# Performance work log

Hardware: AMD Instinct MI355X
Metric: run time of the kernel (lower is better)

Reference implementation:

```python
import math
import jax, jax.numpy as jnp
import numpy as np

B, T, C, H = 2, 4096, 512, 8  # batch, seq_len, n_embd, n_head
D = C // H                    # head_dim = 64

def setup_inputs() -> dict:
    key = jax.random.key(0)
    k1, k2, k3 = jax.random.split(key, 3)
    x = jax.random.normal(k1, (B, T, C), dtype=jnp.float32)
    # torch Linear(C, 3C, bias=False): y = x @ W.T; we store the transposed
    # weight directly so the forward is x @ W_attn.
    W_attn = jax.random.normal(k2, (C, 3 * C), dtype=jnp.float32) * 0.02
    W_proj = jax.random.normal(k3, (C, C), dtype=jnp.float32) * 0.02
    return {"x": x, "W_attn": W_attn, "W_proj": W_proj}

def reference(x, W_attn, W_proj):
    b, t, c = x.shape
    # fused QKV projection, split like .split(n_embd, dim=2)
    qkv = x @ W_attn                              # [B,T,3C]
    q, k, v = jnp.split(qkv, 3, axis=-1)          # each [B,T,C]
    def to_heads(u):
        return u.reshape(b, t, H, D).transpose(0, 2, 1, 3)  # [B,H,T,D]
    q, k, v = to_heads(q), to_heads(k), to_heads(v)
    scale = 1.0 / math.sqrt(D)
    att = jnp.einsum('bhqd,bhkd->bhqk', q, k) * scale       # [B,H,T,T]
    causal = jnp.tril(jnp.ones((t, t), dtype=bool))         # masked_fill(triu(...,1), -inf)
    att = jnp.where(causal, att, -jnp.inf)
    probs = jax.nn.softmax(att, axis=-1)
    y = jnp.einsum('bhqk,bhkd->bhqd', probs, v)             # [B,H,T,D]
    y = y.transpose(0, 2, 1, 3).reshape(b, t, c)            # [B,T,C]
    return y @ W_proj
```

## Files before the change

kernel.cpp:

```cpp
#include <hip/hip_runtime.h>
#include <hip/hip_bf16.h>
#include <stdint.h>


typedef __attribute__((ext_vector_type(8))) short short8;
typedef __attribute__((ext_vector_type(4))) float floatx4;

__device__ __forceinline__ unsigned short f2bf(float f) {
    unsigned int x = __float_as_uint(f);
    unsigned int r = x + 0x7fffu + ((x >> 16) & 1u);
    return (unsigned short)(r >> 16);
}

__device__ __forceinline__ unsigned int pk_bf16(float a, float b) {
    __hip_bfloat162 p = __float22bfloat162_rn(make_float2(a, b));
    return *reinterpret_cast<unsigned int*>(&p);
}

__global__ __launch_bounds__(256) void prep_a(
    const float* __restrict__ x, unsigned short* __restrict__ xb,
    const float* __restrict__ Wa, unsigned short* __restrict__ WaT)
{
    const int bid = blockIdx.x;
    const int tid = threadIdx.x;
    if (bid < 2048) {
        size_t i = ((size_t)bid * 256 + tid) * 8;
        float4 a = *reinterpret_cast<const float4*>(x + i);
        float4 b = *reinterpret_cast<const float4*>(x + i + 4);
        unsigned short o[8] = {f2bf(a.x), f2bf(a.y), f2bf(a.z), f2bf(a.w),
                               f2bf(b.x), f2bf(b.y), f2bf(b.z), f2bf(b.w)};
        *reinterpret_cast<uint4*>(xb + i) = *reinterpret_cast<uint4*>(o);
    } else {
        __shared__ unsigned short tile[32][34];
        const int t2 = bid - 2048;
        const int n0 = (t2 % 48) * 32, k0 = (t2 / 48) * 32;
        const int tx = tid & 31, ty = tid >> 5;
        #pragma unroll
        for (int p = 0; p < 4; ++p)
            tile[tx][ty + p * 8] = f2bf(Wa[(size_t)(k0 + ty + p * 8) * 1536 + n0 + tx]);
        __syncthreads();
        #pragma unroll
        for (int p = 0; p < 4; ++p)
            WaT[(size_t)(n0 + ty + p * 8) * 512 + k0 + tx] = tile[ty + p * 8][tx];
    }
}

__global__ __launch_bounds__(256) void transpose_wp(
    const float* __restrict__ W, unsigned short* __restrict__ Wt)
{
    __shared__ unsigned short tile[32][34];
    const int tid = threadIdx.x;
    const int tx = tid & 31, ty = tid >> 5;
    const int n0 = blockIdx.x * 32, k0 = blockIdx.y * 32;
    #pragma unroll
    for (int p = 0; p < 4; ++p)
        tile[tx][ty + p * 8] = f2bf(W[(size_t)(k0 + ty + p * 8) * 512 + n0 + tx]);
    __syncthreads();
    #pragma unroll
    for (int p = 0; p < 4; ++p)
        Wt[(size_t)(n0 + ty + p * 8) * 512 + k0 + tx] = tile[ty + p * 8][tx];
}

template<int EPI>
__global__ __launch_bounds__(256) void mm_bt(
    const unsigned short* __restrict__ A,
    const unsigned short* __restrict__ Bt,
    void* __restrict__ outp)
{
    __shared__ __align__(16) unsigned char smem[40960];

    const int tid  = threadIdx.x;
    const int wave = tid >> 6;
    const int lane = tid & 63;
    const int quad = lane >> 4;
    const int l16  = lane & 15;
    const int wr   = wave >> 1;
    const int wc   = wave & 1;
    const int m0 = blockIdx.x * 128;
    const int n0 = blockIdx.y * 128;

    floatx4 acc[4][4];
    #pragma unroll
    for (int i = 0; i < 4; ++i)
        #pragma unroll
        for (int j = 0; j < 4; ++j) acc[i][j] = (floatx4){0.f, 0.f, 0.f, 0.f};

    const int row = tid >> 1;
    const int cb  = (tid & 1) * 16;

    const unsigned short* ap = &A[(size_t)(m0 + row) * 512 + cb];
    const unsigned short* bp = &Bt[(size_t)(n0 + row) * 512 + cb];

    uint4 ra0 = *reinterpret_cast<const uint4*>(ap);
    uint4 ra1 = *reinterpret_cast<const uint4*>(ap + 8);
    uint4 rb0 = *reinterpret_cast<const uint4*>(bp);
    uint4 rb1 = *reinterpret_cast<const uint4*>(bp + 8);
    {
        auto Al = reinterpret_cast<unsigned short(*)[40]>(smem);
        auto Bl = reinterpret_cast<unsigned short(*)[40]>(smem + 10240);
        *reinterpret_cast<uint4*>(&Al[row][cb])     = ra0;
        *reinterpret_cast<uint4*>(&Al[row][cb + 8]) = ra1;
        *reinterpret_cast<uint4*>(&Bl[row][cb])     = rb0;
        *reinterpret_cast<uint4*>(&Bl[row][cb + 8]) = rb1;
    }

    for (int it = 0; it < 16; ++it) {
        __syncthreads();
        const int k0 = it * 32;
        if (it < 15) {
            ra0 = *reinterpret_cast<const uint4*>(ap + k0 + 32);
            ra1 = *reinterpret_cast<const uint4*>(ap + k0 + 40);
            rb0 = *reinterpret_cast<const uint4*>(bp + k0 + 32);
            rb1 = *reinterpret_cast<const uint4*>(bp + k0 + 40);
        }

        auto Al = reinterpret_cast<unsigned short(*)[40]>(smem + (it & 1) * 20480);
        auto Bl = reinterpret_cast<unsigned short(*)[40]>(smem + (it & 1) * 20480 + 10240);

        short8 af[4], bf[4];
        #pragma unroll
        for (int ti = 0; ti < 4; ++ti)
            af[ti] = *reinterpret_cast<const short8*>(&Al[wr * 64 + ti * 16 + l16][quad * 8]);
        #pragma unroll
        for (int tj = 0; tj < 4; ++tj)
            bf[tj] = *reinterpret_cast<const short8*>(&Bl[wc * 64 + tj * 16 + l16][quad * 8]);
        #pragma unroll
        for (int ti = 0; ti < 4; ++ti)
            #pragma unroll
            for (int tj = 0; tj < 4; ++tj)
                acc[ti][tj] = __builtin_amdgcn_mfma_f32_16x16x32_bf16(af[ti], bf[tj], acc[ti][tj], 0, 0, 0);

        if (it < 15) {
            auto An = reinterpret_cast<unsigned short(*)[40]>(smem + ((it + 1) & 1) * 20480);
            auto Bn = reinterpret_cast<unsigned short(*)[40]>(smem + ((it + 1) & 1) * 20480 + 10240);
            *reinterpret_cast<uint4*>(&An[row][cb])     = ra0;
            *reinterpret_cast<uint4*>(&An[row][cb + 8]) = ra1;
            *reinterpret_cast<uint4*>(&Bn[row][cb])     = rb0;
            *reinterpret_cast<uint4*>(&Bn[row][cb + 8]) = rb1;
        }
    }

    if (EPI == 0) {
        unsigned short* WS = (unsigned short*)outp;
        unsigned short* Qb  = WS;
        unsigned short* Kb  = WS + 4194304;
        unsigned short* Vtb = WS + 8388608;
        const int which = n0 >> 9;
        const int h = ((n0 + wc * 64) >> 6) & 7;

        if (which == 2) {
            auto Tr = reinterpret_cast<unsigned short(*)[80]>(smem);
            __syncthreads();
            #pragma unroll
            for (int ti = 0; ti < 4; ++ti)
                #pragma unroll
                for (int tj = 0; tj < 4; ++tj) {
                    unsigned int lo = pk_bf16(acc[ti][tj][0], acc[ti][tj][1]);
                    unsigned int hi = pk_bf16(acc[ti][tj][2], acc[ti][tj][3]);
                    *reinterpret_cast<uint2*>(&Tr[(wave << 6) + tj * 16 + l16][ti * 16 + quad * 4])
                        = make_uint2(lo, hi);
                }
            const int b = m0 >> 12;
            const int bh = b * 8 + h;
            const int t0g = (m0 & 4095) + wr * 64;
            const int tseg = (lane & 7) * 8;
            #pragma unroll
            for (int p = 0; p < 8; ++p) {
                int dl = p * 8 + (lane >> 3);
                uint4 v = *reinterpret_cast<const uint4*>(&Tr[(wave << 6) + dl][tseg]);
                *reinterpret_cast<uint4*>(&Vtb[((size_t)(bh * 64 + dl)) * 4096 + t0g + tseg]) = v;
            }
        } else {
            const float sc = (which == 0) ? 0.18033688f : 1.0f;
            #pragma unroll
            for (int ti = 0; ti < 4; ++ti) {
                #pragma unroll
                for (int r = 0; r < 4; ++r) {
                    int m = m0 + wr * 64 + ti * 16 + quad * 4 + r;
                    int b = m >> 12, t = m & 4095;
                    int bh = b * 8 + h;
                    #pragma unroll
                    for (int tj = 0; tj < 4; ++tj) {
                        int d = tj * 16 + l16;
                        unsigned short val = f2bf(acc[ti][tj][r] * sc);
                        if (which == 0) Qb[((size_t)bh * 4096 + t) * 64 + d] = val;
                        else            Kb[((size_t)bh * 4096 + t) * 64 + d] = val;
                    }
                }
            }
        }
    } else {
        float* Out = (float*)outp;
        #pragma unroll
        for (int ti = 0; ti < 4; ++ti) {
            #pragma unroll
            for (int r = 0; r < 4; ++r) {
                int m = m0 + wr * 64 + ti * 16 + quad * 4 + r;
                #pragma unroll
                for (int tj = 0; tj < 4; ++tj) {
                    int n = n0 + wc * 64 + tj * 16 + l16;
                    Out[(size_t)m * 512 + n] = acc[ti][tj][r];
                }
            }
        }
    }
}

__global__ __launch_bounds__(256) void attn_mfma(
    const unsigned short* __restrict__ Q,
    const unsigned short* __restrict__ K,
    const unsigned short* __restrict__ Vt,
    unsigned short* __restrict__ Y)
{
    __shared__ __align__(16) unsigned short Kc[2][64][72];
    __shared__ __align__(16) unsigned short Vc[2][64][72];
    __shared__ __align__(16) unsigned short Pc[4][16][72];

    const int tid  = threadIdx.x;
    const int wave = tid >> 6;
    const int lane = tid & 63;
    const int quad = lane >> 4;
    const int l16  = lane & 15;

    const int bid = blockIdx.x;
    const int bh = bid & 15;
    const int j  = (bid >> 4) & 15;
    const int g  = bid >> 8;
    const int qb = (g == 0) ? j : (g == 1) ? (63 - j) : (g == 2) ? (16 + j) : (47 - j);
    const int m0 = qb * 64;

    const unsigned short* Qp = Q  + (size_t)bh * (4096 * 64);
    const unsigned short* Kp = K  + (size_t)bh * (4096 * 64);
    const unsigned short* Vp = Vt + (size_t)bh * (64 * 4096);

    const int qrow = m0 + wave * 16 + l16;
    short8 qf[2];
    qf[0] = *reinterpret_cast<const short8*>(&Qp[(size_t)qrow * 64 + quad * 8]);
    qf[1] = *reinterpret_cast<const short8*>(&Qp[(size_t)qrow * 64 + 32 + quad * 8]);

    short8 ones;
    #pragma unroll
    for (int i = 0; i < 8; ++i) ones[i] = (short)0x3F80;

    floatx4 o[4] = {{0,0,0,0},{0,0,0,0},{0,0,0,0},{0,0,0,0}};
    floatx4 o4 = {0, 0, 0, 0};

    const int r0 = tid >> 3,          c0 = (tid & 7) * 8;
    const int r1 = (tid + 256) >> 3,  c1 = c0;

    uint4 rk0 = *reinterpret_cast<const uint4*>(&Kp[(size_t)r0 * 64 + c0]);
    uint4 rk1 = *reinterpret_cast<const uint4*>(&Kp[(size_t)r1 * 64 + c1]);
    uint4 rv0 = *reinterpret_cast<const uint4*>(&Vp[(size_t)r0 * 4096 + c0]);
    uint4 rv1 = *reinterpret_cast<const uint4*>(&Vp[(size_t)r1 * 4096 + c1]);
    *reinterpret_cast<uint4*>(&Kc[0][r0][c0]) = rk0;
    *reinterpret_cast<uint4*>(&Kc[0][r1][c1]) = rk1;
    *reinterpret_cast<uint4*>(&Vc[0][r0][c0]) = rv0;
    *reinterpret_cast<uint4*>(&Vc[0][r1][c1]) = rv1;

    for (int kt = 0; kt <= qb; ++kt) {
        __syncthreads();
        const int cur = kt & 1;
        const int nxt = cur ^ 1;

        if (kt < qb) {
            const int jn = (kt + 1) * 64;
            rk0 = *reinterpret_cast<const uint4*>(&Kp[(size_t)(jn + r0) * 64 + c0]);
            rk1 = *reinterpret_cast<const uint4*>(&Kp[(size_t)(jn + r1) * 64 + c1]);
            rv0 = *reinterpret_cast<const uint4*>(&Vp[(size_t)r0 * 4096 + jn + c0]);
            rv1 = *reinterpret_cast<const uint4*>(&Vp[(size_t)r1 * 4096 + jn + c1]);
        }

        float sv[4][4];
        #pragma unroll
        for (int ct = 0; ct < 4; ++ct) {
            floatx4 s = {0, 0, 0, 0};
            #pragma unroll
            for (int kk = 0; kk < 2; ++kk) {
                short8 a = *reinterpret_cast<const short8*>(&Kc[cur][ct * 16 + l16][kk * 32 + quad * 8]);
                s = __builtin_amdgcn_mfma_f32_16x16x32_bf16(a, qf[kk], s, 0, 0, 0);
            }
            sv[ct][0] = s[0]; sv[ct][1] = s[1]; sv[ct][2] = s[2]; sv[ct][3] = s[3];
        }

        if (kt == qb) {
            #pragma unroll
            for (int ct = 0; ct < 4; ++ct)
                #pragma unroll
                for (int r = 0; r < 4; ++r) {
                    int keyl = ct * 16 + quad * 4 + r;
                    int ql   = wave * 16 + l16;
                    sv[ct][r] = (keyl <= ql) ? sv[ct][r] : -1e30f;
                }
        }
        #pragma unroll
        for (int ct = 0; ct < 4; ++ct)
            #pragma unroll
            for (int r = 0; r < 4; ++r)
                sv[ct][r] = __builtin_amdgcn_exp2f(sv[ct][r]);

        #pragma unroll
        for (int ct = 0; ct < 4; ++ct) {
            unsigned int d0 = pk_bf16(sv[ct][0], sv[ct][1]);
            unsigned int d1 = pk_bf16(sv[ct][2], sv[ct][3]);
            *reinterpret_cast<uint2*>(&Pc[wave][l16][ct * 16 + quad * 4]) = make_uint2(d0, d1);
        }

        short8 pa[2];
        pa[0] = *reinterpret_cast<const short8*>(&Pc[wave][l16][quad * 8]);
        pa[1] = *reinterpret_cast<const short8*>(&Pc[wave][l16][32 + quad * 8]);

        #pragma unroll
        for (int kk = 0; kk < 2; ++kk)
            o4 = __builtin_amdgcn_mfma_f32_16x16x32_bf16(pa[kk], ones, o4, 0, 0, 0);
        #pragma unroll
        for (int n = 0; n < 4; ++n) {
            #pragma unroll
            for (int kk = 0; kk < 2; ++kk) {
                short8 b = *reinterpret_cast<const short8*>(&Vc[cur][n * 16 + l16][kk * 32 + quad * 8]);
                o[n] = __builtin_amdgcn_mfma_f32_16x16x32_bf16(pa[kk], b, o[n], 0, 0, 0);
            }
        }

        if (kt < qb) {
            *reinterpret_cast<uint4*>(&Kc[nxt][r0][c0]) = rk0;
            *reinterpret_cast<uint4*>(&Kc[nxt][r1][c1]) = rk1;
            *reinterpret_cast<uint4*>(&Vc[nxt][r0][c0]) = rv0;
            *reinterpret_cast<uint4*>(&Vc[nxt][r1][c1]) = rv1;
        }
    }

    const int b = bh >> 3, h = bh & 7;
    #pragma unroll
    for (int r = 0; r < 4; ++r) {
        float inv = 1.0f / o4[r];
        int t = m0 + wave * 16 + quad * 4 + r;
        #pragma unroll
        for (int n = 0; n < 4; ++n)
            Y[((size_t)(b * 4096 + t)) * 512 + h * 64 + n * 16 + l16] = f2bf(o[n][r] * inv);
    }
}

extern "C" void kernel_launch(void* const* d_in, const int* in_sizes, int n_in,
                              void* d_out, int out_size, void* d_ws, size_t ws_size,
                              hipStream_t stream) {
    const float* x  = (const float*)d_in[0];
    const float* Wa = (const float*)d_in[1];
    const float* Wp = (const float*)d_in[2];
    float* out = (float*)d_out;
    unsigned short* ws = (unsigned short*)d_ws;

    unsigned short* Qb  = ws;
    unsigned short* Kb  = ws + 4194304;
    unsigned short* Vtb = ws + 8388608;
    unsigned short* Yb  = ws + 12582912;
    unsigned short* WaT = Yb;
    unsigned short* WpT = Qb;
    unsigned short* xb  = (unsigned short*)d_out;

    prep_a<<<dim3(2816), dim3(256), 0, stream>>>(x, xb, Wa, WaT);
    mm_bt<0><<<dim3(64, 12), dim3(256), 0, stream>>>(xb, WaT, (void*)ws);
    attn_mfma<<<dim3(1024), dim3(256), 0, stream>>>(Qb, Kb, Vtb, Yb);
    transpose_wp<<<dim3(16, 16), dim3(256), 0, stream>>>(Wp, WpT);
    mm_bt<1><<<dim3(64, 4), dim3(256), 0, stream>>>(Yb, WpT, (void*)out);
}
```

Baseline: 171.8 us.

## Enlarge attention query tile to 128 rows with XOR-swizzled LDS

Each attention block now handles 128 query rows instead of 64: each wave covers two 16-row query tiles, so every K/V tile loaded into LDS is reused across twice as many queries and the grid halves. Padded shared arrays are replaced with unpadded 64-wide rows using an XOR swizzle on the 8-element column chunks to avoid bank conflicts. Waves skip key tiles past their diagonal, which adds divergence between waves in the final tiles and raises register pressure from doubled accumulators. With only 512 blocks, occupancy and load balance across CUs may suffer.

```diff
diff --git a/kernel.cpp b/kernel.cpp
--- a/kernel.cpp
+++ b/kernel.cpp
@@ -212,132 +212,156 @@
     const unsigned short* __restrict__ Vt,
     unsigned short* __restrict__ Y)
 {
-    __shared__ __align__(16) unsigned short Kc[2][64][72];
-    __shared__ __align__(16) unsigned short Vc[2][64][72];
-    __shared__ __align__(16) unsigned short Pc[4][16][72];
+    __shared__ __align__(16) unsigned short Kc[2][64][64];
+    __shared__ __align__(16) unsigned short Vc[2][64][64];
+    __shared__ __align__(16) unsigned short Pc[4][32][64];
 
     const int tid  = threadIdx.x;
     const int wave = tid >> 6;
     const int lane = tid & 63;
     const int quad = lane >> 4;
     const int l16  = lane & 15;
+    const int swz  = l16 & 7;
 
     const int bid = blockIdx.x;
-    const int bh = bid & 15;
-    const int j  = (bid >> 4) & 15;
-    const int g  = bid >> 8;
-    const int qb = (g == 0) ? j : (g == 1) ? (63 - j) : (g == 2) ? (16 + j) : (47 - j);
-    const int m0 = qb * 64;
+    const int bh  = bid & 15;
+    const int j   = (bid >> 4) & 15;
+    const int g   = bid >> 8;
+    const int qb  = (g == 0) ? j : (31 - j);
+    const int m0  = qb * 128;
 
     const unsigned short* Qp = Q  + (size_t)bh * (4096 * 64);
     const unsigned short* Kp = K  + (size_t)bh * (4096 * 64);
     const unsigned short* Vp = Vt + (size_t)bh * (64 * 4096);
 
-    const int qrow = m0 + wave * 16 + l16;
-    short8 qf[2];
-    qf[0] = *reinterpret_cast<const short8*>(&Qp[(size_t)qrow * 64 + quad * 8]);
-    qf[1] = *reinterpret_cast<const short8*>(&Qp[(size_t)qrow * 64 + 32 + quad * 8]);
+    short8 qf[2][2];
+    #pragma unroll
+    for (int qt = 0; qt < 2; ++qt) {
+        const size_t qr = (size_t)(m0 + wave * 32 + qt * 16 + l16) * 64;
+        qf[qt][0] = *reinterpret_cast<const short8*>(&Qp[qr + quad * 8]);
+        qf[qt][1] = *reinterpret_cast<const short8*>(&Qp[qr + 32 + quad * 8]);
+    }
 
     short8 ones;
     #pragma unroll
     for (int i = 0; i < 8; ++i) ones[i] = (short)0x3F80;
 
-    floatx4 o[4] = {{0,0,0,0},{0,0,0,0},{0,0,0,0},{0,0,0,0}};
-    floatx4 o4 = {0, 0, 0, 0};
-
-    const int r0 = tid >> 3,          c0 = (tid & 7) * 8;
-    const int r1 = (tid + 256) >> 3,  c1 = c0;
+    floatx4 o[2][4];
+    #pragma unroll
+    for (int qt = 0; qt < 2; ++qt)
+        #pragma unroll
+        for (int n = 0; n < 4; ++n) o[qt][n] = (floatx4){0.f, 0.f, 0.f, 0.f};
+    floatx4 o4[2] = {{0, 0, 0, 0}, {0, 0, 0, 0}};
+
+    const int r0 = tid >> 3;
+    const int r1 = r0 + 32;
+    const int cc = tid & 7;
+    const int c0 = cc * 8;
+    const int sc = ((cc ^ (r0 & 7)) << 3);
 
     uint4 rk0 = *reinterpret_cast<const uint4*>(&Kp[(size_t)r0 * 64 + c0]);
-    uint4 rk1 = *reinterpret_cast<const uint4*>(&Kp[(size_t)r1 * 64 + c1]);
+    uint4 rk1 = *reinterpret_cast<const uint4*>(&Kp[(size_t)r1 * 64 + c0]);
     uint4 rv0 = *reinterpret_cast<const uint4*>(&Vp[(size_t)r0 * 4096 + c0]);
-    uint4 rv1 = *reinterpret_cast<const uint4*>(&Vp[(size_t)r1 * 4096 + c1]);
-    *reinterpret_cast<uint4*>(&Kc[0][r0][c0]) = rk0;
-    *reinterpret_cast<uint4*>(&Kc[0][r1][c1]) = rk1;
-    *reinterpret_cast<uint4*>(&Vc[0][r0][c0]) = rv0;
-    *reinterpret_cast<uint4*>(&Vc[0][r1][c1]) = rv1;
-
-    for (int kt = 0; kt <= qb; ++kt) {
+    uint4 rv1 = *reinterpret_cast<const uint4*>(&Vp[(size_t)r1 * 4096 + c0]);
+    *reinterpret_cast<uint4*>(&Kc[0][r0][sc]) = rk0;
+    *reinterpret_cast<uint4*>(&Kc[0][r1][sc]) = rk1;
+    *reinterpret_cast<uint4*>(&Vc[0][r0][sc]) = rv0;
+    *reinterpret_cast<uint4*>(&Vc[0][r1][sc]) = rv1;
+
+    const int nt   = 2 * qb + 2;
+    const int diag = 2 * qb + (wave >> 1);
+
+    for (int kt = 0; kt < nt; ++kt) {
         __syncthreads();
         const int cur = kt & 1;
         const int nxt = cur ^ 1;
 
-        if (kt < qb) {
+        if (kt + 1 < nt) {
             const int jn = (kt + 1) * 64;
             rk0 = *reinterpret_cast<const uint4*>(&Kp[(size_t)(jn + r0) * 64 + c0]);
-            rk1 = *reinterpret_cast<const uint4*>(&Kp[(size_t)(jn + r1) * 64 + c1]);
+            rk1 = *reinterpret_cast<const uint4*>(&Kp[(size_t)(jn + r1) * 64 + c0]);
             rv0 = *reinterpret_cast<const uint4*>(&Vp[(size_t)r0 * 4096 + jn + c0]);
-            rv1 = *reinterpret_cast<const uint4*>(&Vp[(size_t)r1 * 4096 + jn + c1]);
-        }
-
-        float sv[4][4];
-        #pragma unroll
-        for (int ct = 0; ct < 4; ++ct) {
-            floatx4 s = {0, 0, 0, 0};
-            #pragma unroll
-            for (int kk = 0; kk < 2; ++kk) {
-                short8 a = *reinterpret_cast<const short8*>(&Kc[cur][ct * 16 + l16][kk * 32 + quad * 8]);
-                s = __builtin_amdgcn_mfma_f32_16x16x32_bf16(a, qf[kk], s, 0, 0, 0);
-            }
-            sv[ct][0] = s[0]; sv[ct][1] = s[1]; sv[ct][2] = s[2]; sv[ct][3] = s[3];
-        }
-
-        if (kt == qb) {
-            #pragma unroll
-            for (int ct = 0; ct < 4; ++ct)
-                #pragma unroll
-                for (int r = 0; r < 4; ++r) {
-                    int keyl = ct * 16 + quad * 4 + r;
-                    int ql   = wave * 16 + l16;
-                    sv[ct][r] = (keyl <= ql) ? sv[ct][r] : -1e30f;
-                }
-        }
-        #pragma unroll
-        for (int ct = 0; ct < 4; ++ct)
-            #pragma unroll
-            for (int r = 0; r < 4; ++r)
-                sv[ct][r] = __builtin_amdgcn_exp2f(sv[ct][r]);
-
-        #pragma unroll
-        for (int ct = 0; ct < 4; ++ct) {
-            unsigned int d0 = pk_bf16(sv[ct][0], sv[ct][1]);
-            unsigned int d1 = pk_bf16(sv[ct][2], sv[ct][3]);
-            *reinterpret_cast<uint2*>(&Pc[wave][l16][ct * 16 + quad * 4]) = make_uint2(d0, d1);
-        }
-
-        short8 pa[2];
-        pa[0] = *reinterpret_cast<const short8*>(&Pc[wave][l16][quad * 8]);
-        pa[1] = *reinterpret_cast<const short8*>(&Pc[wave][l16][32 + quad * 8]);
-
-        #pragma unroll
-        for (int kk = 0; kk < 2; ++kk)
-            o4 = __builtin_amdgcn_mfma_f32_16x16x32_bf16(pa[kk], ones, o4, 0, 0, 0);
-        #pragma unroll
-        for (int n = 0; n < 4; ++n) {
-            #pragma unroll
-            for (int kk = 0; kk < 2; ++kk) {
-                short8 b = *reinterpret_cast<const short8*>(&Vc[cur][n * 16 + l16][kk * 32 + quad * 8]);
-                o[n] = __builtin_amdgcn_mfma_f32_16x16x32_bf16(pa[kk], b, o[n], 0, 0, 0);
-            }
-        }
-
-        if (kt < qb) {
-            *reinterpret_cast<uint4*>(&Kc[nxt][r0][c0]) = rk0;
-            *reinterpret_cast<uint4*>(&Kc[nxt][r1][c1]) = rk1;
-            *reinterpret_cast<uint4*>(&Vc[nxt][r0][c0]) = rv0;
-            *reinterpret_cast<uint4*>(&Vc[nxt][r1][c1]) = rv1;
+            rv1 = *reinterpret_cast<const uint4*>(&Vp[(size_t)r1 * 4096 + jn + c0]);
+        }
+
+        if (kt <= diag) {
+            const bool dg = (kt == diag);
+            #pragma unroll
+            for (int ct = 0; ct < 4; ++ct) {
+                const unsigned short* kr = &Kc[cur][ct * 16 + l16][0];
+                short8 a0 = *reinterpret_cast<const short8*>(kr + ((quad ^ swz) << 3));
+                short8 a1 = *reinterpret_cast<const short8*>(kr + (((4 + quad) ^ swz) << 3));
+                #pragma unroll
+                for (int qt = 0; qt < 2; ++qt) {
+                    floatx4 s = {0, 0, 0, 0};
+                    s = __builtin_amdgcn_mfma_f32_16x16x32_bf16(a0, qf[qt][0], s, 0, 0, 0);
+                    s = __builtin_amdgcn_mfma_f32_16x16x32_bf16(a1, qf[qt][1], s, 0, 0, 0);
+                    float sv[4];
+                    #pragma unroll
+                    for (int r = 0; r < 4; ++r) sv[r] = s[r];
+                    if (dg) {
+                        const int ql = (wave & 1) * 32 + qt * 16 + l16;
+                        #pragma unroll
+                        for (int r = 0; r < 4; ++r) {
+                            int keyl = ct * 16 + quad * 4 + r;
+                            sv[r] = (keyl <= ql) ? sv[r] : -1e30f;
+                        }
+                    }
+                    #pragma unroll
+                    for (int r = 0; r < 4; ++r) sv[r] = __builtin_amdgcn_exp2f(sv[r]);
+                    unsigned int d0 = pk_bf16(sv[0], sv[1]);
+                    unsigned int d1 = pk_bf16(sv[2], sv[3]);
+                    *reinterpret_cast<uint2*>(
+                        &Pc[wave][qt * 16 + l16]
+                           [(((ct * 2 + (quad >> 1)) ^ swz) << 3) + (quad & 1) * 4])
+                        = make_uint2(d0, d1);
+                }
+            }
+
+            short8 pa[2][2];
+            #pragma unroll
+            for (int qt = 0; qt < 2; ++qt) {
+                const unsigned short* pr = &Pc[wave][qt * 16 + l16][0];
+                pa[qt][0] = *reinterpret_cast<const short8*>(pr + ((quad ^ swz) << 3));
+                pa[qt][1] = *reinterpret_cast<const short8*>(pr + (((4 + quad) ^ swz) << 3));
+            }
+            #pragma unroll
+            for (int qt = 0; qt < 2; ++qt) {
+                o4[qt] = __builtin_amdgcn_mfma_f32_16x16x32_bf16(pa[qt][0], ones, o4[qt], 0, 0, 0);
+                o4[qt] = __builtin_amdgcn_mfma_f32_16x16x32_bf16(pa[qt][1], ones, o4[qt], 0, 0, 0);
+            }
+            #pragma unroll
+            for (int n = 0; n < 4; ++n) {
+                const unsigned short* vr = &Vc[cur][n * 16 + l16][0];
+                short8 b0 = *reinterpret_cast<const short8*>(vr + ((quad ^ swz) << 3));
+                short8 b1 = *reinterpret_cast<const short8*>(vr + (((4 + quad) ^ swz) << 3));
+                #pragma unroll
+                for (int qt = 0; qt < 2; ++qt) {
+                    o[qt][n] = __builtin_amdgcn_mfma_f32_16x16x32_bf16(pa[qt][0], b0, o[qt][n], 0, 0, 0);
+                    o[qt][n] = __builtin_amdgcn_mfma_f32_16x16x32_bf16(pa[qt][1], b1, o[qt][n], 0, 0, 0);
+                }
+            }
+        }
+
+        if (kt + 1 < nt) {
+            *reinterpret_cast<uint4*>(&Kc[nxt][r0][sc]) = rk0;
+            *reinterpret_cast<uint4*>(&Kc[nxt][r1][sc]) = rk1;
+            *reinterpret_cast<uint4*>(&Vc[nxt][r0][sc]) = rv0;
+            *reinterpret_cast<uint4*>(&Vc[nxt][r1][sc]) = rv1;
         }
     }
 
     const int b = bh >> 3, h = bh & 7;
     #pragma unroll
-    for (int r = 0; r < 4; ++r) {
-        float inv = 1.0f / o4[r];
-        int t = m0 + wave * 16 + quad * 4 + r;
-        #pragma unroll
-        for (int n = 0; n < 4; ++n)
-            Y[((size_t)(b * 4096 + t)) * 512 + h * 64 + n * 16 + l16] = f2bf(o[n][r] * inv);
-    }
+    for (int qt = 0; qt < 2; ++qt)
+        #pragma unroll
+        for (int r = 0; r < 4; ++r) {
+            float inv = 1.0f / o4[qt][r];
+            int t = m0 + wave * 32 + qt * 16 + quad * 4 + r;
+            #pragma unroll
+            for (int n = 0; n < 4; ++n)
+                Y[((size_t)(b * 4096 + t)) * 512 + h * 64 + n * 16 + l16] = f2bf(o[qt][n][r] * inv);
+        }
 }
 
 extern "C" void kernel_launch(void* const* d_in, const int* in_sizes, int n_in,
@@ -359,7 +383,7 @@
 
     prep_a<<<dim3(2816), dim3(256), 0, stream>>>(x, xb, Wa, WaT);
     mm_bt<0><<<dim3(64, 12), dim3(256), 0, stream>>>(xb, WaT, (void*)ws);
-    attn_mfma<<<dim3(1024), dim3(256), 0, stream>>>(Qb, Kb, Vtb, Yb);
+    attn_mfma<<<dim3(512), dim3(256), 0, stream>>>(Qb, Kb, Vtb, Yb);
     transpose_wp<<<dim3(16, 16), dim3(256), 0, stream>>>(Wp, WpT);
     mm_bt<1><<<dim3(64, 4), dim3(256), 0, stream>>>(Yb, WpT, (void*)out);
 }
```

Result: slower. 176.9 us (+3.0%).

## Rework attention with 32x32 MFMA, paired causal blocks, swizzled LDS, register P

Applied to the files above, without the earlier changes.

The attention kernel now uses 32x32x16 bf16 MFMA tiles and each wave owns 32 query rows. Each block pairs a low and a high query block so causal work is balanced across blocks, which halves the grid. K/V shared tiles use an XOR swizzle instead of padding, and P is rearranged in registers with permlane32 swap (or shuffles as a fallback) instead of going through LDS. The row sum is accumulated on the bf16-rounded probabilities instead of with an extra ones-MFMA. In exchange, waves handling the low block sit idle for the later iterations while still joining the shared K/V loads, and the larger accumulators raise register pressure.

```diff
diff --git a/kernel.cpp b/kernel.cpp
--- a/kernel.cpp
+++ b/kernel.cpp
@@ -5,6 +5,13 @@
 
 typedef __attribute__((ext_vector_type(8))) short short8;
 typedef __attribute__((ext_vector_type(4))) float floatx4;
+typedef __attribute__((ext_vector_type(16))) float floatx16;
+#if __has_builtin(__builtin_amdgcn_permlane32_swap)
+typedef __attribute__((ext_vector_type(2))) unsigned int uint2v;
+#define HAVE_PLSWAP 1
+#else
+#define HAVE_PLSWAP 0
+#endif
 
 __device__ __forceinline__ unsigned short f2bf(float f) {
     unsigned int x = __float_as_uint(f);
@@ -15,6 +22,10 @@
 __device__ __forceinline__ unsigned int pk_bf16(float a, float b) {
     __hip_bfloat162 p = __float22bfloat162_rn(make_float2(a, b));
     return *reinterpret_cast<unsigned int*>(&p);
+}
+
+__device__ __forceinline__ float bfsum2(unsigned int w) {
+    return __uint_as_float(w << 16) + __uint_as_float(w & 0xffff0000u);
 }
 
 __global__ __launch_bounds__(256) void prep_a(
@@ -212,131 +223,172 @@
     const unsigned short* __restrict__ Vt,
     unsigned short* __restrict__ Y)
 {
-    __shared__ __align__(16) unsigned short Kc[2][64][72];
-    __shared__ __align__(16) unsigned short Vc[2][64][72];
-    __shared__ __align__(16) unsigned short Pc[4][16][72];
+    __shared__ __align__(16) unsigned short Kc[2][64][64];
+    __shared__ __align__(16) unsigned short Vc[2][64][64];
+    __shared__ __align__(16) float Ws[4][32];
 
     const int tid  = threadIdx.x;
     const int wave = tid >> 6;
     const int lane = tid & 63;
-    const int quad = lane >> 4;
-    const int l16  = lane & 15;
+    const int l32  = lane & 31;
+    const int hh   = lane >> 5;
+    const int sw7  = lane & 7;
 
     const int bid = blockIdx.x;
-    const int bh = bid & 15;
-    const int j  = (bid >> 4) & 15;
-    const int g  = bid >> 8;
-    const int qb = (g == 0) ? j : (g == 1) ? (63 - j) : (g == 2) ? (16 + j) : (47 - j);
-    const int m0 = qb * 64;
+    const int bh  = bid & 15;
+    const int u   = (bid >> 4) & 15;
+    const int ilo = (bid >> 8) ? (31 - u) : u;
+    const int ihi = 63 - ilo;
+    const int qbw = (wave < 2) ? ilo : ihi;
+    const int qg0 = qbw * 64 + (wave & 1) * 32;
 
     const unsigned short* Qp = Q  + (size_t)bh * (4096 * 64);
     const unsigned short* Kp = K  + (size_t)bh * (4096 * 64);
     const unsigned short* Vp = Vt + (size_t)bh * (64 * 4096);
 
-    const int qrow = m0 + wave * 16 + l16;
-    short8 qf[2];
-    qf[0] = *reinterpret_cast<const short8*>(&Qp[(size_t)qrow * 64 + quad * 8]);
-    qf[1] = *reinterpret_cast<const short8*>(&Qp[(size_t)qrow * 64 + 32 + quad * 8]);
-
-    short8 ones;
-    #pragma unroll
-    for (int i = 0; i < 8; ++i) ones[i] = (short)0x3F80;
-
-    floatx4 o[4] = {{0,0,0,0},{0,0,0,0},{0,0,0,0},{0,0,0,0}};
-    floatx4 o4 = {0, 0, 0, 0};
-
-    const int r0 = tid >> 3,          c0 = (tid & 7) * 8;
-    const int r1 = (tid + 256) >> 3,  c1 = c0;
-
-    uint4 rk0 = *reinterpret_cast<const uint4*>(&Kp[(size_t)r0 * 64 + c0]);
-    uint4 rk1 = *reinterpret_cast<const uint4*>(&Kp[(size_t)r1 * 64 + c1]);
-    uint4 rv0 = *reinterpret_cast<const uint4*>(&Vp[(size_t)r0 * 4096 + c0]);
-    uint4 rv1 = *reinterpret_cast<const uint4*>(&Vp[(size_t)r1 * 4096 + c1]);
-    *reinterpret_cast<uint4*>(&Kc[0][r0][c0]) = rk0;
-    *reinterpret_cast<uint4*>(&Kc[0][r1][c1]) = rk1;
-    *reinterpret_cast<uint4*>(&Vc[0][r0][c0]) = rv0;
-    *reinterpret_cast<uint4*>(&Vc[0][r1][c1]) = rv1;
-
-    for (int kt = 0; kt <= qb; ++kt) {
+    short8 qf[4];
+    #pragma unroll
+    for (int k16 = 0; k16 < 4; ++k16)
+        qf[k16] = *reinterpret_cast<const short8*>(
+            &Qp[(size_t)(qg0 + l32) * 64 + k16 * 16 + hh * 8]);
+
+    floatx16 o0 = {0,0,0,0,0,0,0,0,0,0,0,0,0,0,0,0};
+    floatx16 o1 = {0,0,0,0,0,0,0,0,0,0,0,0,0,0,0,0};
+    float rs = 0.f;
+
+    const int rr  = tid >> 3;
+    const int cc  = tid & 7;
+    const int c0  = cc * 8;
+    const int scs = ((cc ^ (rr & 7)) << 3);
+
+    uint4 rk0 = *reinterpret_cast<const uint4*>(&Kp[(size_t)rr * 64 + c0]);
+    uint4 rk1 = *reinterpret_cast<const uint4*>(&Kp[(size_t)(rr + 32) * 64 + c0]);
+    uint4 rv0 = *reinterpret_cast<const uint4*>(&Vp[(size_t)rr * 4096 + c0]);
+    uint4 rv1 = *reinterpret_cast<const uint4*>(&Vp[(size_t)(rr + 32) * 4096 + c0]);
+    *reinterpret_cast<uint4*>(&Kc[0][rr][scs])      = rk0;
+    *reinterpret_cast<uint4*>(&Kc[0][rr + 32][scs]) = rk1;
+    *reinterpret_cast<uint4*>(&Vc[0][rr][scs])      = rv0;
+    *reinterpret_cast<uint4*>(&Vc[0][rr + 32][scs]) = rv1;
+
+    const int NT = ihi + 1;
+    for (int kt = 0; kt < NT; ++kt) {
         __syncthreads();
         const int cur = kt & 1;
         const int nxt = cur ^ 1;
 
-        if (kt < qb) {
+        if (kt + 1 < NT) {
             const int jn = (kt + 1) * 64;
-            rk0 = *reinterpret_cast<const uint4*>(&Kp[(size_t)(jn + r0) * 64 + c0]);
-            rk1 = *reinterpret_cast<const uint4*>(&Kp[(size_t)(jn + r1) * 64 + c1]);
-            rv0 = *reinterpret_cast<const uint4*>(&Vp[(size_t)r0 * 4096 + jn + c0]);
-            rv1 = *reinterpret_cast<const uint4*>(&Vp[(size_t)r1 * 4096 + jn + c1]);
-        }
-
-        float sv[4][4];
-        #pragma unroll
-        for (int ct = 0; ct < 4; ++ct) {
-            floatx4 s = {0, 0, 0, 0};
-            #pragma unroll
-            for (int kk = 0; kk < 2; ++kk) {
-                short8 a = *reinterpret_cast<const short8*>(&Kc[cur][ct * 16 + l16][kk * 32 + quad * 8]);
-                s = __builtin_amdgcn_mfma_f32_16x16x32_bf16(a, qf[kk], s, 0, 0, 0);
-            }
-            sv[ct][0] = s[0]; sv[ct][1] = s[1]; sv[ct][2] = s[2]; sv[ct][3] = s[3];
-        }
-
-        if (kt == qb) {
-            #pragma unroll
-            for (int ct = 0; ct < 4; ++ct)
+            rk0 = *reinterpret_cast<const uint4*>(&Kp[(size_t)(jn + rr) * 64 + c0]);
+            rk1 = *reinterpret_cast<const uint4*>(&Kp[(size_t)(jn + rr + 32) * 64 + c0]);
+            rv0 = *reinterpret_cast<const uint4*>(&Vp[(size_t)rr * 4096 + jn + c0]);
+            rv1 = *reinterpret_cast<const uint4*>(&Vp[(size_t)(rr + 32) * 4096 + jn + c0]);
+        }
+
+        if (kt <= qbw) {
+            floatx16 s0 = {0,0,0,0,0,0,0,0,0,0,0,0,0,0,0,0};
+            floatx16 s1 = {0,0,0,0,0,0,0,0,0,0,0,0,0,0,0,0};
+            #pragma unroll
+            for (int k16 = 0; k16 < 4; ++k16) {
+                const int chs = ((k16 * 2 + hh) ^ sw7) << 3;
+                short8 a0 = *reinterpret_cast<const short8*>(&Kc[cur][l32][chs]);
+                short8 a1 = *reinterpret_cast<const short8*>(&Kc[cur][32 + l32][chs]);
+                s0 = __builtin_amdgcn_mfma_f32_32x32x16_bf16(a0, qf[k16], s0, 0, 0, 0);
+                s1 = __builtin_amdgcn_mfma_f32_32x32x16_bf16(a1, qf[k16], s1, 0, 0, 0);
+            }
+            if (kt == qbw) {
+                const int ql = (wave & 1) * 32 + l32;
                 #pragma unroll
-                for (int r = 0; r < 4; ++r) {
-                    int keyl = ct * 16 + quad * 4 + r;
-                    int ql   = wave * 16 + l16;
-                    sv[ct][r] = (keyl <= ql) ? sv[ct][r] : -1e30f;
+                for (int r = 0; r < 16; ++r) {
+                    const int kl = (r & 3) + 8 * (r >> 2) + 4 * hh;
+                    s0[r] = (kl      <= ql) ? s0[r] : -1e30f;
+                    s1[r] = (kl + 32 <= ql) ? s1[r] : -1e30f;
                 }
-        }
-        #pragma unroll
-        for (int ct = 0; ct < 4; ++ct)
-            #pragma unroll
-            for (int r = 0; r < 4; ++r)
-                sv[ct][r] = __builtin_amdgcn_exp2f(sv[ct][r]);
-
-        #pragma unroll
-        for (int ct = 0; ct < 4; ++ct) {
-            unsigned int d0 = pk_bf16(sv[ct][0], sv[ct][1]);
-            unsigned int d1 = pk_bf16(sv[ct][2], sv[ct][3]);
-            *reinterpret_cast<uint2*>(&Pc[wave][l16][ct * 16 + quad * 4]) = make_uint2(d0, d1);
-        }
-
-        short8 pa[2];
-        pa[0] = *reinterpret_cast<const short8*>(&Pc[wave][l16][quad * 8]);
-        pa[1] = *reinterpret_cast<const short8*>(&Pc[wave][l16][32 + quad * 8]);
-
-        #pragma unroll
-        for (int kk = 0; kk < 2; ++kk)
-            o4 = __builtin_amdgcn_mfma_f32_16x16x32_bf16(pa[kk], ones, o4, 0, 0, 0);
-        #pragma unroll
-        for (int n = 0; n < 4; ++n) {
-            #pragma unroll
-            for (int kk = 0; kk < 2; ++kk) {
-                short8 b = *reinterpret_cast<const short8*>(&Vc[cur][n * 16 + l16][kk * 32 + quad * 8]);
-                o[n] = __builtin_amdgcn_mfma_f32_16x16x32_bf16(pa[kk], b, o[n], 0, 0, 0);
-            }
-        }
-
-        if (kt < qb) {
-            *reinterpret_cast<uint4*>(&Kc[nxt][r0][c0]) = rk0;
-            *reinterpret_cast<uint4*>(&Kc[nxt][r1][c1]) = rk1;
-            *reinterpret_cast<uint4*>(&Vc[nxt][r0][c0]) = rv0;
-            *reinterpret_cast<uint4*>(&Vc[nxt][r1][c1]) = rv1;
-        }
-    }
+            }
+            #pragma unroll
+            for (int r = 0; r < 16; ++r) {
+                s0[r] = __builtin_amdgcn_exp2f(s0[r]);
+                s1[r] = __builtin_amdgcn_exp2f(s1[r]);
+            }
+
+            short8 pa[4];
+            #pragma unroll
+            for (int t = 0; t < 2; ++t) {
+                float e0  = t ? s1[0]  : s0[0],  e1  = t ? s1[1]  : s0[1];
+                float e2  = t ? s1[2]  : s0[2],  e3  = t ? s1[3]  : s0[3];
+                float e4  = t ? s1[4]  : s0[4],  e5  = t ? s1[5]  : s0[5];
+                float e6  = t ? s1[6]  : s0[6],  e7  = t ? s1[7]  : s0[7];
+                float e8  = t ? s1[8]  : s0[8],  e9  = t ? s1[9]  : s0[9];
+                float e10 = t ? s1[10] : s0[10], e11 = t ? s1[11] : s0[11];
+                float e12 = t ? s1[12] : s0[12], e13 = t ? s1[13] : s0[13];
+                float e14 = t ? s1[14] : s0[14], e15 = t ? s1[15] : s0[15];
+                unsigned int A0 = pk_bf16(e0, e1),   B0 = pk_bf16(e2, e3);
+                unsigned int A1 = pk_bf16(e4, e5),   B1 = pk_bf16(e6, e7);
+                unsigned int A2 = pk_bf16(e8, e9),   B2 = pk_bf16(e10, e11);
+                unsigned int A3 = pk_bf16(e12, e13), B3 = pk_bf16(e14, e15);
+                rs += bfsum2(A0) + bfsum2(B0) + bfsum2(A1) + bfsum2(B1)
+                    + bfsum2(A2) + bfsum2(B2) + bfsum2(A3) + bfsum2(B3);
+#if HAVE_PLSWAP
+                uint2v rA = __builtin_amdgcn_permlane32_swap(A0, A1, false, false);
+                uint2v rB = __builtin_amdgcn_permlane32_swap(B0, B1, false, false);
+                uint4 u0 = make_uint4(rA[0], rB[0], rA[1], rB[1]);
+                pa[t * 2] = *reinterpret_cast<short8*>(&u0);
+                rA = __builtin_amdgcn_permlane32_swap(A2, A3, false, false);
+                rB = __builtin_amdgcn_permlane32_swap(B2, B3, false, false);
+                uint4 u1 = make_uint4(rA[0], rB[0], rA[1], rB[1]);
+                pa[t * 2 + 1] = *reinterpret_cast<short8*>(&u1);
+#else
+                unsigned int pA0 = __shfl_xor((int)A0, 32), pA1 = __shfl_xor((int)A1, 32);
+                unsigned int pB0 = __shfl_xor((int)B0, 32), pB1 = __shfl_xor((int)B1, 32);
+                unsigned int pA2 = __shfl_xor((int)A2, 32), pA3 = __shfl_xor((int)A3, 32);
+                unsigned int pB2 = __shfl_xor((int)B2, 32), pB3 = __shfl_xor((int)B3, 32);
+                uint4 u0 = make_uint4(hh ? pA1 : A0, hh ? pB1 : B0,
+                                      hh ? A1 : pA0, hh ? B1 : pB0);
+                pa[t * 2] = *reinterpret_cast<short8*>(&u0);
+                uint4 u1 = make_uint4(hh ? pA3 : A2, hh ? pB3 : B2,
+                                      hh ? A3 : pA2, hh ? B3 : pB2);
+                pa[t * 2 + 1] = *reinterpret_cast<short8*>(&u1);
+#endif
+            }
+
+            #pragma unroll
+            for (int f = 0; f < 4; ++f) {
+                const int chs = ((f * 2 + hh) ^ sw7) << 3;
+                short8 b0 = *reinterpret_cast<const short8*>(&Vc[cur][l32][chs]);
+                short8 b1 = *reinterpret_cast<const short8*>(&Vc[cur][32 + l32][chs]);
+                o0 = __builtin_amdgcn_mfma_f32_32x32x16_bf16(pa[f], b0, o0, 0, 0, 0);
+                o1 = __builtin_amdgcn_mfma_f32_32x32x16_bf16(pa[f], b1, o1, 0, 0, 0);
+            }
+        }
+
+        if (kt + 1 < NT) {
+            *reinterpret_cast<uint4*>(&Kc[nxt][rr][scs])      = rk0;
+            *reinterpret_cast<uint4*>(&Kc[nxt][rr + 32][scs]) = rk1;
+            *reinterpret_cast<uint4*>(&Vc[nxt][rr][scs])      = rv0;
+            *reinterpret_cast<uint4*>(&Vc[nxt][rr + 32][scs]) = rv1;
+        }
+    }
+
+    float tot = rs + __shfl_xor(rs, 32);
+    if (lane < 32) Ws[wave][l32] = 1.0f / tot;
+    __syncthreads();
+
+    float4 iv[4];
+    #pragma unroll
+    for (int g = 0; g < 4; ++g)
+        iv[g] = *reinterpret_cast<const float4*>(&Ws[wave][g * 8 + hh * 4]);
 
     const int b = bh >> 3, h = bh & 7;
     #pragma unroll
-    for (int r = 0; r < 4; ++r) {
-        float inv = 1.0f / o4[r];
-        int t = m0 + wave * 16 + quad * 4 + r;
-        #pragma unroll
-        for (int n = 0; n < 4; ++n)
-            Y[((size_t)(b * 4096 + t)) * 512 + h * 64 + n * 16 + l16] = f2bf(o[n][r] * inv);
+    for (int g = 0; g < 4; ++g) {
+        #pragma unroll
+        for (int rsub = 0; rsub < 4; ++rsub) {
+            const int r = g * 4 + rsub;
+            const int t = qg0 + 8 * g + 4 * hh + rsub;
+            const float sc = iv[g][rsub];
+            unsigned short* yr = &Y[((size_t)(b * 4096 + t)) * 512 + h * 64];
+            yr[l32]      = f2bf(o0[r] * sc);
+            yr[32 + l32] = f2bf(o1[r] * sc);
+        }
     }
 }
 
@@ -359,7 +411,7 @@
 
     prep_a<<<dim3(2816), dim3(256), 0, stream>>>(x, xb, Wa, WaT);
     mm_bt<0><<<dim3(64, 12), dim3(256), 0, stream>>>(xb, WaT, (void*)ws);
-    attn_mfma<<<dim3(1024), dim3(256), 0, stream>>>(Qb, Kb, Vtb, Yb);
+    attn_mfma<<<dim3(512), dim3(256), 0, stream>>>(Qb, Kb, Vtb, Yb);
     transpose_wp<<<dim3(16, 16), dim3(256), 0, stream>>>(Wp, WpT);
     mm_bt<1><<<dim3(64, 4), dim3(256), 0, stream>>>(Yb, WpT, (void*)out);
 }
```

Result: slower. 187.8 us (+9.3%).
